# Optimization experiments

Measured on AMD Instinct MI355X. Metric: run time of the kernel, lower is better.

The kernel has to match this reference:

```python
import jax, jax.numpy as jnp
import numpy as np

B, C, D, H = 128, 8, 1024, 8
K_RANGE = (2, 3, 4, 5)


def setup_inputs() -> dict:
    key = jax.random.key(0)
    ks = jax.random.split(key, 10)
    s = 0.02
    return {
        "x": jax.random.normal(ks[0], (B, D), jnp.float32),
        # per-K prototype groups, shape (nb_classes, K, embed_dim) as in get_prototype_group()
        "p2": jax.random.normal(ks[1], (C, 2, D), jnp.float32),
        "p3": jax.random.normal(ks[2], (C, 3, D), jnp.float32),
        "p4": jax.random.normal(ks[3], (C, 4, D), jnp.float32),
        "p5": jax.random.normal(ks[4], (C, 5, D), jnp.float32),
        # per-class attention Block params (stacked over class axis)
        "ln_g": jnp.ones((C, D), jnp.float32),
        "ln_b": jnp.zeros((C, D), jnp.float32),
        "w_qkv": jax.random.normal(ks[5], (C, 3 * D, D), jnp.float32) * s,
        "b_qkv": jnp.zeros((C, 3 * D), jnp.float32),
        "w_proj": jax.random.normal(ks[6], (C, D, D), jnp.float32) * s,
        "b_proj": jnp.zeros((C, D), jnp.float32),
        # cls head
        "w_cls": jax.random.normal(ks[7], (C, D), jnp.float32) * s,
        "b_cls": jnp.zeros((C,), jnp.float32),
    }


def _proto_group(x, pg):
    """x: (B,D); pg: (C,K,D). Returns nearest proto (B,D), per-sample class group (B,K,D), class ids (B,)."""
    Cc, K, d = pg.shape
    flat = pg.reshape(Cc * K, d)
    # squared L2 distances (argmin identical to torch.cdist p=2 argmin)
    d2 = (jnp.sum(x * x, axis=1, keepdims=True)
          - 2.0 * (x @ flat.T)
          + jnp.sum(flat * flat, axis=1))
    idx = jnp.argmin(d2, axis=1)          # (B,)
    cls = idx // K                        # (B,)
    return flat[idx], pg[cls], cls


def _vicreg(x, nearest, proto_space, sim_c=25.0, std_c=25.0, cov_c=1.0):
    # sim: pull x toward its nearest prototype in every K-group
    repr_loss = jnp.mean((x[:, None, :] - nearest) ** 2)
    # std over batch of prototype space, unbiased var, eps=1e-4
    std = jnp.sqrt(jnp.var(proto_space, axis=0, ddof=1) + 1e-4)   # (S,D)
    std_loss = jnp.mean(jax.nn.relu(1.0 - std))
    # covariance of centered flattened prototype space
    ps = proto_space - jnp.mean(proto_space, axis=0)
    P = ps.reshape(-1, ps.shape[-1])                              # (B*S, D)
    cov = P.T @ P / (P.shape[0] - 1)
    cov_loss = ((cov ** 2).sum() - (jnp.diagonal(cov) ** 2).sum()) / ps.shape[-1]
    return sim_c * repr_loss + std_c * std_loss + cov_c * cov_loss


def _forward(x, p2, p3, p4, p5, ln_g, ln_b, w_qkv, b_qkv, w_proj, b_proj, w_cls, b_cls):
    groups = (p2, p3, p4, p5)
    nearest_list, space_list, cls = [], [], None
    for pg in groups:
        n, sp, cls = _proto_group(x, pg)   # cls kept from LAST group, as in torch code
        nearest_list.append(n)
        space_list.append(sp)
    nearest = jnp.stack(nearest_list, axis=1)     # (B, len(K_range), D)
    proto_space = jnp.concatenate(space_list, 1)  # (B, sum(K_range), D)

    vcr = _vicreg(x, nearest, proto_space)

    # per-class attention Block: LayerNorm -> MHA -> residual, vectorized over class axis c
    S = proto_space.shape[1]
    mu = proto_space.mean(-1, keepdims=True)
    var = proto_space.var(-1, keepdims=True)
    xn = (proto_space - mu) * jax.lax.rsqrt(var + 1e-5)               # (B,S,D)
    h = xn[None] * ln_g[:, None, None, :] + ln_b[:, None, None, :]    # (C,B,S,D)

    qkv = jnp.einsum('cbsd,cfd->cbsf', h, w_qkv) + b_qkv[:, None, None, :]
    dh = D // H
    qkv = qkv.reshape(C, B, S, 3, H, dh).transpose(3, 0, 1, 4, 2, 5)  # (3,C,B,H,S,dh)
    q, k, v = qkv[0] * (dh ** -0.5), qkv[1], qkv[2]
    attn = jax.nn.softmax(jnp.einsum('cbhqe,cbhke->cbhqk', q, k), axis=-1)
    o = jnp.einsum('cbhqk,cbhke->cbhqe', attn, v)                     # (C,B,H,S,dh)
    o = o.transpose(0, 1, 3, 2, 4).reshape(C, B, S, D)
    out = jnp.einsum('cbsd,ced->cbse', o, w_proj) + b_proj[:, None, None, :]
    attended = proto_space[None] + out                                # (C,B,S,D)

    # route each sample through the block of its (last-group) assigned class
    cond = attended[cls, jnp.arange(B)]                               # (B,S,D)
    cond = cond / jnp.maximum(jnp.linalg.norm(cond, axis=2, keepdims=True), 1e-12)
    pooled = cond.mean(1)                                             # (B,D)
    logits = pooled @ w_cls.T + b_cls
    return logits, vcr


def reference(x, p2, p3, p4, p5, ln_g, ln_b, w_qkv, b_qkv, w_proj, b_proj, w_cls, b_cls):
    return _forward(x, p2, p3, p4, p5, ln_g, ln_b, w_qkv, b_qkv, w_proj, b_proj, w_cls, b_cls)
```

## Files before the change

kernel.cpp:

```cpp
#include <hip/hip_runtime.h>
#include <math.h>

#define NB 128
#define ND 1024
#define NS 14
#define NDH 128

typedef float f32x4 __attribute__((ext_vector_type(4)));
typedef short bf16x8 __attribute__((ext_vector_type(8)));
typedef unsigned int u32x4 __attribute__((ext_vector_type(4)));

__device__ __forceinline__ unsigned short f2bf(float v) {
  unsigned int u = __builtin_bit_cast(unsigned int, v);
  return (unsigned short)((u + 0x7FFFu + ((u >> 16) & 1u)) >> 16);
}
__device__ __forceinline__ float bf2f(unsigned short u) {
  return __builtin_bit_cast(float, (unsigned int)u << 16);
}

__device__ __forceinline__ bf16x8 pack_bv(float4 w0, float4 w1) {
  unsigned int u0, u1, u2, u3;
  asm("v_cvt_pk_bf16_f32 %0, %1, %2" : "=v"(u0) : "v"(w0.x), "v"(w0.y));
  asm("v_cvt_pk_bf16_f32 %0, %1, %2" : "=v"(u1) : "v"(w0.z), "v"(w0.w));
  asm("v_cvt_pk_bf16_f32 %0, %1, %2" : "=v"(u2) : "v"(w1.x), "v"(w1.y));
  asm("v_cvt_pk_bf16_f32 %0, %1, %2" : "=v"(u3) : "v"(w1.z), "v"(w1.w));
  u32x4 u = {u0, u1, u2, u3};
  return __builtin_bit_cast(bf16x8, u);
}

__device__ __forceinline__ void s_decomp(int s, int& g, int& k) {
  if (s < 2)      { g = 0; k = s; }
  else if (s < 5) { g = 1; k = s - 2; }
  else if (s < 9) { g = 2; k = s - 5; }
  else            { g = 3; k = s - 9; }
}
__device__ __forceinline__ const float* grp_ptr(int g, const float* p2, const float* p3,
                                                const float* p4, const float* p5) {
  return g == 0 ? p2 : g == 1 ? p3 : g == 2 ? p4 : p5;
}
__device__ __forceinline__ int grp_base(int g) { return g == 0 ? 0 : g == 1 ? 16 : g == 2 ? 40 : 72; }
__device__ __forceinline__ int grp_k(int g) { return g + 2; }

__global__ __launch_bounds__(256) void k_ln_assign(
    const float* __restrict__ x,
    const float* __restrict__ p2, const float* __restrict__ p3,
    const float* __restrict__ p4, const float* __restrict__ p5,
    const float* __restrict__ ln_g, const float* __restrict__ ln_b,
    unsigned short* __restrict__ hbf2, float* __restrict__ pall,
    int* __restrict__ cls, int* __restrict__ rows_g, float* __restrict__ minv)
{
  int bid = blockIdx.x, t = threadIdx.x;
  __shared__ __align__(16) float xs[ND];
  float4* xs4 = (float4*)xs;
  if (bid < 112) {
    int r = bid;
    const float* pp; int idx;
    if (r < 16)      { pp = p2; idx = r; }
    else if (r < 40) { pp = p3; idx = r - 16; }
    else if (r < 72) { pp = p4; idx = r - 40; }
    else             { pp = p5; idx = r - 72; }
    const float4* row4 = (const float4*)(pp + (size_t)idx * ND);
    float4 v = row4[t];
    xs4[t] = v;
    float s1 = v.x + v.y + v.z + v.w;
    float s2 = v.x * v.x + v.y * v.y + v.z * v.z + v.w * v.w;
    __shared__ float ra[256], rb[256];
    ra[t] = s1; rb[t] = s2; __syncthreads();
    for (int o = 128; o > 0; o >>= 1) { if (t < o) { ra[t] += ra[t + o]; rb[t] += rb[t + o]; } __syncthreads(); }
    __shared__ float mu, rstd;
    if (t == 0) {
      float m = ra[0] * (1.f / 1024.f);
      float var = rb[0] * (1.f / 1024.f) - m * m;
      mu = m; rstd = rsqrtf(var + 1e-5f);
    }
    __syncthreads();
    ((float4*)(pall + (size_t)r * ND))[t] = xs4[t];
    float4 xv = xs4[t];
    float nx = (xv.x - mu) * rstd, ny = (xv.y - mu) * rstd,
          nz = (xv.z - mu) * rstd, nw = (xv.w - mu) * rstd;
    int d0 = t * 4;
    int m = r >> 4, rr = r & 15;
    int kblk = d0 >> 5, qq = (d0 >> 3) & 3, e0 = d0 & 7;
    size_t fidx = (size_t)kblk * 3584 + m * 512 + (qq * 16 + rr) * 8 + e0;
#pragma unroll
    for (int c = 0; c < 8; ++c) {
      float4 g = ((const float4*)(ln_g + (size_t)c * ND))[t];
      float4 bb = ((const float4*)(ln_b + (size_t)c * ND))[t];
      ushort4 u;
      u.x = f2bf(nx * g.x + bb.x); u.y = f2bf(ny * g.y + bb.y);
      u.z = f2bf(nz * g.z + bb.z); u.w = f2bf(nw * g.w + bb.w);
      *(ushort4*)&hbf2[(size_t)c * 114688 + fidx] = u;
    }
  } else {
    int b = bid - 112;
    __shared__ float d2s[112];
    __shared__ int cls_s[4];
    const float4* xg4 = (const float4*)(x + (size_t)b * ND);
    xs4[t] = xg4[t];
    __syncthreads();
    int j = t >> 1, half = t & 1;
    if (j < 112) {
      const float* pp; int idx;
      if (j < 16)      { pp = p2; idx = j; }
      else if (j < 40) { pp = p3; idx = j - 16; }
      else if (j < 72) { pp = p4; idx = j - 40; }
      else             { pp = p5; idx = j - 72; }
      const float4* pr4 = (const float4*)(pp + (size_t)idx * ND);
      float acc = 0.f;
      int d0 = half * 128;
#pragma unroll 8
      for (int d = d0; d < d0 + 128; ++d) {
        float4 a = xs4[d], p = pr4[d];
        float dx = a.x - p.x, dy = a.y - p.y, dz = a.z - p.z, dw = a.w - p.w;
        acc += dx * dx + dy * dy + dz * dz + dw * dw;
      }
      acc += __shfl_xor(acc, 1, 2);
      if (half == 0) d2s[j] = acc;
    }
    __syncthreads();
    if (t < 4) {
      int base = grp_base(t), kg = grp_k(t), cnt = 8 * kg;
      float mv = d2s[base]; int mi = 0;
      for (int jj = 1; jj < cnt; ++jj) { float v = d2s[base + jj]; if (v < mv) { mv = v; mi = jj; } }
      int c = mi / kg;
      cls[b * 4 + t] = c; cls_s[t] = c;
      minv[b * 4 + t] = mv;
    }
    __syncthreads();
    if (t < NS) {
      int g, k; s_decomp(t, g, k);
      rows_g[b * NS + t] = grp_base(g) + cls_s[g] * grp_k(g) + k;
    }
  }
}

__global__ __launch_bounds__(256, 4) void k_qkv_prep(
    const unsigned short* __restrict__ hbf2, const float* __restrict__ w_qkv,
    const float* __restrict__ b_qkv, unsigned short* __restrict__ qkv_bf,
    const int* __restrict__ cls, const float* __restrict__ minv,
    int* __restrict__ counts, int* __restrict__ ccnt, int* __restrict__ order,
    int* __restrict__ posof, int* __restrict__ chunkidx, int* __restrict__ chunk_c,
    int* __restrict__ chunk_lo, int* __restrict__ chunkN, float* __restrict__ scal)
{
  int bid = blockIdx.x, t = threadIdx.x;
  if (bid == 0) {
    __shared__ int cnt_s[32];
    __shared__ int cc_s[8];
    __shared__ float red[128];
    if (t < 32) cnt_s[t] = 0;
    if (t < 8) cc_s[t] = 0;
    if (t < 4) scal[t] = 0.f;
    __syncthreads();
    if (t < 128) {
      int c3;
#pragma unroll
      for (int g = 0; g < 4; ++g) {
        int c = cls[t * 4 + g];
        atomicAdd(&cnt_s[g * 8 + c], 1);
        if (g == 3) c3 = c;
      }
      int pos = atomicAdd(&cc_s[c3], 1);
      order[c3 * 128 + pos] = t;
      posof[t] = pos;
      red[t] = minv[t * 4 + 0] + minv[t * 4 + 1] + minv[t * 4 + 2] + minv[t * 4 + 3];
    }
    __syncthreads();
    for (int o = 64; o > 0; o >>= 1) { if (t < o) red[t] += red[t + o]; __syncthreads(); }
    if (t == 0) {
      scal[0] = red[0];
      int T = 0;
      for (int c = 0; c < 8; ++c) {
        chunkidx[c] = T;
        int nch = (cc_s[c] + 15) >> 4;
        for (int j = 0; j < nch; ++j) { chunk_c[T] = c; chunk_lo[T] = j * 16; ++T; }
      }
      chunkN[0] = T;
    }
    if (t < 32) counts[t] = cnt_s[t];
    if (t < 8) ccnt[t] = cc_s[t];
    return;
  }
  __shared__ __align__(16) float lred[3 * 14 * 256];
  int qb = bid - 1;
  int c = qb / 96, xb = qb - c * 96;
  int lane = t & 63, ks = t >> 6;
  int r16 = lane & 15, q = lane >> 4;
  int col0 = xb * 32 + r16, col1 = col0 + 16;
  const float* Wp0 = w_qkv + ((size_t)c * 3072 + col0) * ND + ks * 256 + q * 8;
  const float* Wp1 = Wp0 + (size_t)16 * ND;
  const unsigned short* Hp = hbf2 + (size_t)c * 114688 + (size_t)(ks * 8) * 3584 + lane * 8;
  f32x4 acc0[7] = {}, acc1[7] = {};
#pragma unroll
  for (int i = 0; i < 8; ++i) {
    float4 w00 = *(const float4*)(Wp0 + i * 32);
    float4 w01 = *(const float4*)(Wp0 + i * 32 + 4);
    float4 w10 = *(const float4*)(Wp1 + i * 32);
    float4 w11 = *(const float4*)(Wp1 + i * 32 + 4);
    bf16x8 av[7];
#pragma unroll
    for (int m = 0; m < 7; ++m) av[m] = *(const bf16x8*)(Hp + (size_t)i * 3584 + m * 512);
    bf16x8 bv0 = pack_bv(w00, w01);
    bf16x8 bv1 = pack_bv(w10, w11);
#pragma unroll
    for (int m = 0; m < 7; ++m) {
      acc0[m] = __builtin_amdgcn_mfma_f32_16x16x32_bf16(av[m], bv0, acc0[m], 0, 0, 0);
      acc1[m] = __builtin_amdgcn_mfma_f32_16x16x32_bf16(av[m], bv1, acc1[m], 0, 0, 0);
    }
  }
  if (ks) {
#pragma unroll
    for (int m = 0; m < 7; ++m) {
      *(f32x4*)&lred[((ks - 1) * 14 + m) * 256 + lane * 4] = acc0[m];
      *(f32x4*)&lred[((ks - 1) * 14 + 7 + m) * 256 + lane * 4] = acc1[m];
    }
  }
  __syncthreads();
  if (ks == 0) {
    float bq0 = b_qkv[(size_t)c * 3072 + col0];
    float bq1 = b_qkv[(size_t)c * 3072 + col1];
#pragma unroll
    for (int m = 0; m < 7; ++m) {
      f32x4 s0 = acc0[m], s1 = acc1[m];
#pragma unroll
      for (int sk = 0; sk < 3; ++sk) {
        s0 += *(const f32x4*)&lred[(sk * 14 + m) * 256 + lane * 4];
        s1 += *(const f32x4*)&lred[(sk * 14 + 7 + m) * 256 + lane * 4];
      }
#pragma unroll
      for (int r = 0; r < 4; ++r) {
        int row = m * 16 + q * 4 + r;
        qkv_bf[((size_t)c * 112 + row) * 3072 + col0] = f2bf(s0[r] + bq0);
        qkv_bf[((size_t)c * 112 + row) * 3072 + col1] = f2bf(s1[r] + bq1);
      }
    }
  }
}

__global__ __launch_bounds__(256) void k_attn_stats(
    const unsigned short* __restrict__ qkv_bf, const int* __restrict__ cls,
    const int* __restrict__ rows_g, const int* __restrict__ posof,
    const int* __restrict__ chunkidx, unsigned short* __restrict__ obf2,
    const float* __restrict__ p2, const float* __restrict__ p3,
    const float* __restrict__ p4, const float* __restrict__ p5,
    const int* __restrict__ counts, float* __restrict__ M, float* __restrict__ scal)
{
  int bid = blockIdx.x, t = threadIdx.x;
  if (bid < 1024) {
    __shared__ __align__(16) float qs[NS * NDH], ks2[NS * NDH], vs[NS * NDH];
    __shared__ float sc[NS * NS];
    __shared__ int rg[NS];
    int h = bid & 7, b = bid >> 3;
    if (t < NS) rg[t] = rows_g[b * NS + t];
    __syncthreads();
    int cp = cls[b * 4 + 3];
    int pos = posof[b];
    size_t gbase = (size_t)(chunkidx[cp] + (pos >> 4)) * 229376;
    int slot = pos & 15;
    const float scale = 0.08838834764831843f;
    for (int i = t; i < NS * 32; i += 256) {
      int s = i >> 5, e4 = (i & 31) * 4;
      size_t base = ((size_t)cp * 112 + rg[s]) * 3072 + h * NDH + e4;
      ushort4 uq = *(const ushort4*)&qkv_bf[base];
      ushort4 uk = *(const ushort4*)&qkv_bf[base + 1024];
      ushort4 uv = *(const ushort4*)&qkv_bf[base + 2048];
      int o = s * NDH + e4;
      qs[o]     = bf2f(uq.x) * scale; qs[o + 1] = bf2f(uq.y) * scale;
      qs[o + 2] = bf2f(uq.z) * scale; qs[o + 3] = bf2f(uq.w) * scale;
      ks2[o]     = bf2f(uk.x); ks2[o + 1] = bf2f(uk.y);
      ks2[o + 2] = bf2f(uk.z); ks2[o + 3] = bf2f(uk.w);
      vs[o]     = bf2f(uv.x); vs[o + 1] = bf2f(uv.y);
      vs[o + 2] = bf2f(uv.z); vs[o + 3] = bf2f(uv.w);
    }
    __syncthreads();
    if (t < NS * NS) {
      int si = t / NS, sj = t - (t / NS) * NS;
      const float4* qa = (const float4*)&qs[si * NDH];
      const float4* kb = (const float4*)&ks2[sj * NDH];
      float acc = 0.f;
#pragma unroll 8
      for (int e4 = 0; e4 < 32; ++e4) {
        float4 a = qa[e4], k4 = kb[e4];
        acc += a.x * k4.x + a.y * k4.y + a.z * k4.z + a.w * k4.w;
      }
      sc[t] = acc;
    }
    __syncthreads();
    if (t < NS) {
      float mx = -1e30f;
      for (int j = 0; j < NS; ++j) mx = fmaxf(mx, sc[t * NS + j]);
      float e_[NS]; float sum = 0.f;
      for (int j = 0; j < NS; ++j) { float e = expf(sc[t * NS + j] - mx); e_[j] = e; sum += e; }
      float inv = 1.f / sum;
      for (int j = 0; j < NS; ++j) sc[t * NS + j] = e_[j] * inv;
    }
    __syncthreads();
    for (int i = t; i < NS * 32; i += 256) {
      int s = i >> 5, e4 = i & 31;
      float4 a = {0.f, 0.f, 0.f, 0.f};
#pragma unroll
      for (int j = 0; j < NS; ++j) {
        float w = sc[s * NS + j];
        float4 v4 = ((const float4*)&vs[j * NDH])[e4];
        a.x += w * v4.x; a.y += w * v4.y; a.z += w * v4.z; a.w += w * v4.w;
      }
      int row = slot * 14 + s;
      int m = row >> 4, r16 = row & 15;
      int d0 = h * NDH + e4 * 4;
      int kblk = d0 >> 5, qq = (d0 >> 3) & 3, e0 = d0 & 7;
      ushort4 u; u.x = f2bf(a.x); u.y = f2bf(a.y); u.z = f2bf(a.z); u.w = f2bf(a.w);
      *(ushort4*)&obf2[gbase + (size_t)kblk * 7168 + m * 512 + (qq * 16 + r16) * 8 + e0] = u;
    }
  } else {
    int idx = (bid - 1024) * 256 + t;
    int s = idx >> 10, d = idx & 1023;
    int g, k; s_decomp(s, g, k);
    const float* pp = grp_ptr(g, p2, p3, p4, p5);
    int kg = grp_k(g);
    float vc[8], nc[8];
    float sum = 0.f, sumsq = 0.f;
#pragma unroll
    for (int c = 0; c < 8; ++c) {
      float v = pp[((size_t)(c * kg + k)) * ND + d];
      float n = (float)counts[g * 8 + c];
      vc[c] = v; nc[c] = n;
      sum += n * v; sumsq += n * v * v;
    }
    float mean = sum * (1.f / 128.f);
    float var = (sumsq - 128.f * mean * mean) * (1.f / 127.f);
    float sd = sqrtf(var + 1e-4f);
#pragma unroll
    for (int c = 0; c < 8; ++c)
      M[((size_t)(s * 8 + c)) * ND + d] = sqrtf(nc[c] * (1.f / 1791.f)) * (vc[c] - mean);
    float part = fmaxf(1.f - sd, 0.f);
    __shared__ float red[256];
    red[t] = part; __syncthreads();
    for (int o = 128; o > 0; o >>= 1) { if (t < o) red[t] += red[t + o]; __syncthreads(); }
    if (t == 0) atomicAdd(&scal[1], red[0]);
  }
}

__global__ __launch_bounds__(512) void k_proj_gram(
    const unsigned short* __restrict__ obf2, const int* __restrict__ order,
    const int* __restrict__ ccnt, const int* __restrict__ chunk_c,
    const int* __restrict__ chunk_lo, const int* __restrict__ chunkN,
    const int* __restrict__ rows_g,
    const float* __restrict__ w_proj, const float* __restrict__ b_proj,
    const float* __restrict__ pall, float* __restrict__ att,
    const float* __restrict__ M, float* __restrict__ scal)
{
  int bid = blockIdx.x, t = threadIdx.x;
  if (bid < 960) {
    int g = bid / 64, xb = bid - g * 64;
    if (g >= chunkN[0]) return;
    __shared__ __align__(16) float lred[3 * 2 * 7 * 256];
    __shared__ int sid_s[16];
    int c = chunk_c[g], lo = chunk_lo[g];
    int cnt = ccnt[c];
    int nb = cnt - lo; if (nb > 16) nb = 16;
    int lane = t & 63, wid = t >> 6;
    int rh = wid & 1, ks = wid >> 1;
    if (t < 16) sid_s[t] = order[c * 128 + lo + ((t < nb) ? t : nb - 1)];
    int r16 = lane & 15, q = lane >> 4;
    int col = xb * 16 + r16;
    const float* Wp = w_proj + ((size_t)c * ND + col) * ND + ks * 256 + q * 8;
    const unsigned short* Ap = obf2 + (size_t)g * 229376 + (size_t)(ks * 8) * 7168 + rh * 3584 + lane * 8;
    f32x4 acc[7] = {};
#pragma unroll
    for (int i = 0; i < 8; ++i) {
      float4 w0 = *(const float4*)(Wp + i * 32);
      float4 w1 = *(const float4*)(Wp + i * 32 + 4);
      bf16x8 bv = pack_bv(w0, w1);
      const unsigned short* ak = Ap + (size_t)i * 7168;
#pragma unroll
      for (int m = 0; m < 7; ++m) {
        bf16x8 av = *(const bf16x8*)(ak + m * 512);
        acc[m] = __builtin_amdgcn_mfma_f32_16x16x32_bf16(av, bv, acc[m], 0, 0, 0);
      }
    }
    if (ks) {
#pragma unroll
      for (int m = 0; m < 7; ++m)
        *(f32x4*)&lred[(((ks - 1) * 2 + rh) * 7 + m) * 256 + lane * 4] = acc[m];
    }
    __syncthreads();
    if (ks == 0) {
      float bp = b_proj[(size_t)c * ND + col];
#pragma unroll
      for (int m = 0; m < 7; ++m) {
        f32x4 a1 = *(const f32x4*)&lred[((0 * 2 + rh) * 7 + m) * 256 + lane * 4];
        f32x4 a2 = *(const f32x4*)&lred[((1 * 2 + rh) * 7 + m) * 256 + lane * 4];
        f32x4 a3 = *(const f32x4*)&lred[((2 * 2 + rh) * 7 + m) * 256 + lane * 4];
#pragma unroll
        for (int r = 0; r < 4; ++r) {
          int row = rh * 112 + m * 16 + q * 4 + r;
          int slot = row / 14, s = row - slot * 14;
          if (slot < nb) {
            int b = sid_s[slot];
            float res = pall[(size_t)rows_g[b * NS + s] * ND + col];
            att[((size_t)b * NS + s) * ND + col] = acc[m][r] + a1[r] + a2[r] + a3[r] + bp + res;
          }
        }
      }
    }
  } else if (bid < 1072) {
    int r = bid - 960;
    __shared__ __align__(16) float mi[ND];
    __shared__ float red2[128];
    float4* mi4 = (float4*)mi;
    const float4* src4 = (const float4*)(M + (size_t)r * ND);
    if (t < 256) mi4[t] = src4[t];
    if (t < 128) red2[t] = 0.f;
    __syncthreads();
    int j = t >> 2, qd = t & 3;
    float p = 0.f;
    if (j < 112) {
      const float4* mj4 = (const float4*)(M + (size_t)j * ND);
      float acc = 0.f;
#pragma unroll 8
      for (int d = qd * 64; d < qd * 64 + 64; ++d) {
        float4 a = mi4[d], b = mj4[d];
        acc += a.x * b.x + a.y * b.y + a.z * b.z + a.w * b.w;
      }
      acc += __shfl_xor(acc, 1, 4);
      acc += __shfl_xor(acc, 2, 4);
      p = acc * acc;
    }
    if (qd == 0 && j < 112) red2[j] = p;
    __syncthreads();
    for (int o = 64; o > 0; o >>= 1) { if (t < o) red2[t] += red2[t + o]; __syncthreads(); }
    if (t == 0) atomicAdd(&scal[2], red2[0]);
  } else {
    int d = (bid - 1072) * 512 + t;
    float tsum = 0.f;
    for (int r = 0; r < 112; ++r) { float v = M[(size_t)r * ND + d]; tsum += v * v; }
    __shared__ float red3[512];
    red3[t] = tsum * tsum; __syncthreads();
    for (int o = 256; o > 0; o >>= 1) { if (t < o) red3[t] += red3[t + o]; __syncthreads(); }
    if (t == 0) atomicAdd(&scal[3], red3[0]);
  }
}

__global__ __launch_bounds__(256) void k_final(
    const float* __restrict__ att, const float* __restrict__ w_cls,
    const float* __restrict__ b_cls, const float* __restrict__ scal,
    float* __restrict__ out)
{
  int b = blockIdx.x, t = threadIdx.x;
  __shared__ __align__(16) float as[NS * ND];
  __shared__ float wred[NS][4];
  __shared__ float inv[NS];
  __shared__ __align__(16) float pooled[ND];
  int lane = t & 63, w = t >> 6;
#pragma unroll
  for (int s = 0; s < NS; ++s) {
    float4 v = ((const float4*)(att + ((size_t)b * NS + s) * ND))[t];
    ((float4*)&as[s * ND])[t] = v;
    float p = v.x * v.x + v.y * v.y + v.z * v.z + v.w * v.w;
#pragma unroll
    for (int o = 32; o > 0; o >>= 1) p += __shfl_xor(p, o, 64);
    if (lane == 0) wred[s][w] = p;
  }
  __syncthreads();
  if (t < NS) {
    float s2 = wred[t][0] + wred[t][1] + wred[t][2] + wred[t][3];
    inv[t] = 1.f / fmaxf(sqrtf(s2), 1e-12f);
  }
  __syncthreads();
  float4 pa = {0.f, 0.f, 0.f, 0.f};
#pragma unroll
  for (int s = 0; s < NS; ++s) {
    float iv = inv[s];
    float4 v = ((const float4*)&as[s * ND])[t];
    pa.x += iv * v.x; pa.y += iv * v.y; pa.z += iv * v.z; pa.w += iv * v.w;
  }
  const float k14 = 1.f / 14.f;
  pa.x *= k14; pa.y *= k14; pa.z *= k14; pa.w *= k14;
  ((float4*)pooled)[t] = pa;
  __syncthreads();
  int c = t >> 5, l = t & 31;
  float acc = 0.f;
#pragma unroll
  for (int k = 0; k < 8; ++k) {
    int i4 = l + k * 32;
    float4 p4 = ((const float4*)pooled)[i4];
    float4 wc = ((const float4*)(w_cls + (size_t)c * ND))[i4];
    acc += p4.x * wc.x + p4.y * wc.y + p4.z * wc.z + p4.w * wc.w;
  }
  for (int o = 16; o > 0; o >>= 1) acc += __shfl_down(acc, o, 32);
  if (l == 0) out[b * 8 + c] = acc + b_cls[c];
  if (b == 0 && t == 0) {
    float repr = scal[0] * (1.f / (128.f * 4.f * 1024.f));
    float stdl = scal[1] * (1.f / 14336.f);
    float covl = (scal[2] - scal[3]) * (1.f / 1024.f);
    out[1024] = 25.f * repr + 25.f * stdl + covl;
  }
}

extern "C" void kernel_launch(void* const* d_in, const int* in_sizes, int n_in,
                              void* d_out, int out_size, void* d_ws, size_t ws_size,
                              hipStream_t stream) {
  const float* x      = (const float*)d_in[0];
  const float* p2     = (const float*)d_in[1];
  const float* p3     = (const float*)d_in[2];
  const float* p4     = (const float*)d_in[3];
  const float* p5     = (const float*)d_in[4];
  const float* ln_g   = (const float*)d_in[5];
  const float* ln_b   = (const float*)d_in[6];
  const float* w_qkv  = (const float*)d_in[7];
  const float* b_qkv  = (const float*)d_in[8];
  const float* w_proj = (const float*)d_in[9];
  const float* b_proj = (const float*)d_in[10];
  const float* w_cls  = (const float*)d_in[11];
  const float* b_cls  = (const float*)d_in[12];
  float* out = (float*)d_out;
  char* ws = (char*)d_ws;

  float* scal      = (float*)(ws + 0);
  int*   counts    = (int*)(ws + 64);
  int*   ccnt      = (int*)(ws + 192);
  int*   cls       = (int*)(ws + 256);
  int*   rows_g    = (int*)(ws + 2304);
  int*   order     = (int*)(ws + 9472);
  float* minv      = (float*)(ws + 13568);
  int*   posof     = (int*)(ws + 15616);
  int*   chunkidx  = (int*)(ws + 16128);
  int*   chunk_c   = (int*)(ws + 16160);
  int*   chunk_lo  = (int*)(ws + 16224);
  int*   chunkN    = (int*)(ws + 16288);
  float* pall      = (float*)(ws + 16384);
  unsigned short* hbf2 = (unsigned short*)(ws + 475136);
  unsigned short* qkvb = (unsigned short*)(ws + 2310144);
  unsigned short* obf2 = (unsigned short*)(ws + 7815168);
  float* att       = (float*)(ws + 15155200);
  float* M         = (float*)(ws + 22495232);

  k_ln_assign<<<240, 256, 0, stream>>>(x, p2, p3, p4, p5, ln_g, ln_b, hbf2, pall, cls, rows_g, minv);
  k_qkv_prep<<<769, 256, 0, stream>>>(hbf2, w_qkv, b_qkv, qkvb, cls, minv,
                                      counts, ccnt, order, posof, chunkidx, chunk_c, chunk_lo, chunkN, scal);
  k_attn_stats<<<1080, 256, 0, stream>>>(qkvb, cls, rows_g, posof, chunkidx, obf2,
                                         p2, p3, p4, p5, counts, M, scal);
  k_proj_gram<<<1074, 512, 0, stream>>>(obf2, order, ccnt, chunk_c, chunk_lo, chunkN, rows_g,
                                        w_proj, b_proj, pall, att, M, scal);
  k_final<<<128, 256, 0, stream>>>(att, w_cls, b_cls, scal, out);
}
```

Measured before the change: 119.0 us.

## Pre-convert w_proj to bf16 MFMA fragment layout in first kernel

Adds 4096 extra blocks to the first kernel that convert the whole w_proj weight tensor to bf16 and write it in an MFMA-fragment-ordered layout in the workspace. The projection GEMM then loads one contiguous bf16x8 per lane instead of two fp32 float4 loads plus a pack, which halves its weight read volume. The trade-off is a full extra pass over w_proj (fp32 read plus bf16 write) in the earlier kernel. Because this conversion runs on every call and every weight chunk is re-read by the GEMM, the total traffic may not drop.

After: 120.5 us. Within noise of the previous version (+1.3%).

```diff
diff --git a/kernel.cpp b/kernel.cpp
--- a/kernel.cpp
+++ b/kernel.cpp
@@ -46,10 +46,25 @@
     const float* __restrict__ p2, const float* __restrict__ p3,
     const float* __restrict__ p4, const float* __restrict__ p5,
     const float* __restrict__ ln_g, const float* __restrict__ ln_b,
+    const float* __restrict__ w_proj, unsigned short* __restrict__ wpf,
     unsigned short* __restrict__ hbf2, float* __restrict__ pall,
     int* __restrict__ cls, int* __restrict__ rows_g, float* __restrict__ minv)
 {
   int bid = blockIdx.x, t = threadIdx.x;
+  if (bid >= 240) {
+    int idxT = (bid - 240) * 256 + t;
+    int c = idxT >> 17;
+    int rem = idxT & 131071;
+    int col = rem >> 7, kq = rem & 127;
+    const float* src = w_proj + (((size_t)c * 1024 + col) << 10) + kq * 8;
+    float4 w0 = *(const float4*)(src);
+    float4 w1 = *(const float4*)(src + 4);
+    bf16x8 v = pack_bv(w0, w1);
+    size_t dst = ((((size_t)c * 64 + (col >> 4)) * 32 + (kq >> 2)) << 9)
+               + ((kq & 3) * 16 + (col & 15)) * 8;
+    *(bf16x8*)(wpf + dst) = v;
+    return;
+  }
   __shared__ __align__(16) float xs[ND];
   float4* xs4 = (float4*)xs;
   if (bid < 112) {
@@ -340,11 +355,12 @@
 }
 
 __global__ __launch_bounds__(512) void k_proj_gram(
-    const unsigned short* __restrict__ obf2, const int* __restrict__ order,
+    const unsigned short* __restrict__ obf2, const unsigned short* __restrict__ wpf,
+    const int* __restrict__ order,
     const int* __restrict__ ccnt, const int* __restrict__ chunk_c,
     const int* __restrict__ chunk_lo, const int* __restrict__ chunkN,
     const int* __restrict__ rows_g,
-    const float* __restrict__ w_proj, const float* __restrict__ b_proj,
+    const float* __restrict__ b_proj,
     const float* __restrict__ pall, float* __restrict__ att,
     const float* __restrict__ M, float* __restrict__ scal)
 {
@@ -362,14 +378,12 @@
     if (t < 16) sid_s[t] = order[c * 128 + lo + ((t < nb) ? t : nb - 1)];
     int r16 = lane & 15, q = lane >> 4;
     int col = xb * 16 + r16;
-    const float* Wp = w_proj + ((size_t)c * ND + col) * ND + ks * 256 + q * 8;
+    const unsigned short* Wf = wpf + ((((size_t)c * 64 + xb) * 32 + ks * 8) << 9) + lane * 8;
     const unsigned short* Ap = obf2 + (size_t)g * 229376 + (size_t)(ks * 8) * 7168 + rh * 3584 + lane * 8;
     f32x4 acc[7] = {};
 #pragma unroll
     for (int i = 0; i < 8; ++i) {
-      float4 w0 = *(const float4*)(Wp + i * 32);
-      float4 w1 = *(const float4*)(Wp + i * 32 + 4);
-      bf16x8 bv = pack_bv(w0, w1);
+      bf16x8 bv = *(const bf16x8*)(Wf + (size_t)i * 512);
       const unsigned short* ak = Ap + (size_t)i * 7168;
 #pragma unroll
       for (int m = 0; m < 7; ++m) {
@@ -533,13 +547,15 @@
   unsigned short* obf2 = (unsigned short*)(ws + 7815168);
   float* att       = (float*)(ws + 15155200);
   float* M         = (float*)(ws + 22495232);
-
-  k_ln_assign<<<240, 256, 0, stream>>>(x, p2, p3, p4, p5, ln_g, ln_b, hbf2, pall, cls, rows_g, minv);
+  unsigned short* wpf = (unsigned short*)(ws + 22953984);
+
+  k_ln_assign<<<4336, 256, 0, stream>>>(x, p2, p3, p4, p5, ln_g, ln_b, w_proj, wpf,
+                                        hbf2, pall, cls, rows_g, minv);
   k_qkv_prep<<<769, 256, 0, stream>>>(hbf2, w_qkv, b_qkv, qkvb, cls, minv,
                                       counts, ccnt, order, posof, chunkidx, chunk_c, chunk_lo, chunkN, scal);
   k_attn_stats<<<1080, 256, 0, stream>>>(qkvb, cls, rows_g, posof, chunkidx, obf2,
                                          p2, p3, p4, p5, counts, M, scal);
-  k_proj_gram<<<1074, 512, 0, stream>>>(obf2, order, ccnt, chunk_c, chunk_lo, chunkN, rows_g,
-                                        w_proj, b_proj, pall, att, M, scal);
+  k_proj_gram<<<1074, 512, 0, stream>>>(obf2, wpf, order, ccnt, chunk_c, chunk_lo, chunkN, rows_g,
+                                        b_proj, pall, att, M, scal);
   k_final<<<128, 256, 0, stream>>>(att, w_cls, b_cls, scal, out);
 }
```
